# Performance work log

Hardware: AMD Instinct MI355X
Metric: run time of the kernel (lower is better)

## Reference

```python
import jax, jax.numpy as jnp
import numpy as np

H = W = 224
WS = 7          # window size
SS = 3          # shift size
NH = 12         # num heads
N = WS * WS     # tokens per window (49)


def _attn_mask():
    # shift-window attention mask, computed from static ints (numpy)
    img = np.zeros((H, W), np.float32)
    cnt = 0
    for h0, h1 in [(0, H - WS), (H - WS, H - SS), (H - SS, H)]:
        for w0, w1 in [(0, W - WS), (W - WS, W - SS), (W - SS, W)]:
            img[h0:h1, w0:w1] = cnt
            cnt += 1
    mw = img.reshape(H // WS, WS, W // WS, WS).transpose(0, 2, 1, 3).reshape(-1, N)
    diff = mw[:, None, :] - mw[:, :, None]          # (nW, N, N)
    m = np.where(diff != 0, -100.0, 0.0).astype(np.float32)
    return m[:, None, :, :]                         # (nW, 1, N, N)


def _rel_pos_index():
    coords = np.stack(np.meshgrid(np.arange(WS), np.arange(WS), indexing='ij'))
    cf = coords.reshape(2, -1)
    rc = (cf[:, :, None] - cf[:, None, :]).transpose(1, 2, 0)  # (N, N, 2)
    rc[..., 0] += WS - 1
    rc[..., 1] += WS - 1
    rc[..., 0] *= 2 * WS - 1
    return rc.sum(-1).reshape(-1)                    # (N*N,)


_MASK = _attn_mask()
_RPI = _rel_pos_index()


def _ln(x, w, b, eps=1e-5):
    mu = jnp.mean(x, -1, keepdims=True)
    var = jnp.mean((x - mu) ** 2, -1, keepdims=True)
    return (x - mu) / jnp.sqrt(var + eps) * w + b


def setup_inputs() -> dict:
    key = jax.random.key(0)
    ks = jax.random.split(key, 12)
    C, CM = 384, 1536
    s = 0.02
    return {
        'x': jax.random.normal(ks[0], (1, H * W, C), jnp.float32),
        'rpb_table': jax.random.normal(ks[1], (169, NH), jnp.float32) * s,
        'qkv_w': jax.random.normal(ks[2], (3 * C, C), jnp.float32) * s,
        'qkv_b': jax.random.normal(ks[3], (3 * C,), jnp.float32) * s,
        'proj_w': jax.random.normal(ks[4], (C, C), jnp.float32) * s,
        'proj_b': jax.random.normal(ks[5], (C,), jnp.float32) * s,
        'fc1_w': jax.random.normal(ks[6], (CM, C), jnp.float32) * s,
        'fc1_b': jax.random.normal(ks[7], (CM,), jnp.float32) * s,
        'fc2_w': jax.random.normal(ks[8], (C, CM), jnp.float32) * s,
        'fc2_b': jax.random.normal(ks[9], (C,), jnp.float32) * s,
        'norm1_w': jnp.ones((C,), jnp.float32),
        'norm1_b': jnp.zeros((C,), jnp.float32),
        'norm2_w': jnp.ones((C,), jnp.float32),
        'norm2_b': jnp.zeros((C,), jnp.float32),
    }


def reference(x, rpb_table, qkv_w, qkv_b, proj_w, proj_b, fc1_w, fc1_b,
              fc2_w, fc2_b, norm1_w, norm1_b, norm2_w, norm2_b):
    B, L, C = x.shape
    hd = C // NH
    scale = hd ** -0.5
    mask = jnp.asarray(_MASK)                        # (nW, 1, N, N)
    rpi = jnp.asarray(_RPI)

    shortcut = x
    h = _ln(x, norm1_w, norm1_b).reshape(B, H, W, C)
    h = jnp.roll(h, (-SS, -SS), axis=(1, 2))
    # window partition -> (B*nW, N, C)
    win = h.reshape(B, H // WS, WS, W // WS, WS, C).transpose(0, 1, 3, 2, 4, 5)
    win = win.reshape(-1, N, C)

    qkv = (win @ qkv_w.T + qkv_b).reshape(-1, N, 3, NH, hd).transpose(2, 0, 3, 1, 4)
    q, k, v = qkv[0] * scale, qkv[1], qkv[2]         # (nW, NH, N, hd)
    attn = jnp.einsum('whnd,whmd->whnm', q, k)
    bias = rpb_table[rpi].reshape(N, N, NH).transpose(2, 0, 1)[None]  # (1, NH, N, N)
    attn = jax.nn.softmax(attn + bias + mask, axis=-1)
    out = jnp.einsum('whnm,whmd->whnd', attn, v).transpose(0, 2, 1, 3).reshape(-1, N, C)
    out = out @ proj_w.T + proj_b

    # window reverse + unshift
    h = out.reshape(B, H // WS, W // WS, WS, WS, C).transpose(0, 1, 3, 2, 4, 5)
    h = h.reshape(B, H, W, C)
    h = jnp.roll(h, (SS, SS), axis=(1, 2)).reshape(B, L, C)

    x = shortcut + h
    y = _ln(x, norm2_w, norm2_b)
    y = jax.nn.gelu(y @ fc1_w.T + fc1_b, approximate=False)  # torch nn.GELU = erf
    y = y @ fc2_w.T + fc2_b
    return x + y
```

## Files before the change

### kernel.cpp

```cpp
#include <hip/hip_runtime.h>
#include <cstdint>
#include <cstddef>

#define AS1 __attribute__((address_space(1)))
#define AS3 __attribute__((address_space(3)))

typedef __attribute__((ext_vector_type(8))) short bf16x8;
typedef __attribute__((ext_vector_type(4))) short short4v;
typedef __attribute__((ext_vector_type(8))) unsigned short u16x8;
typedef __attribute__((ext_vector_type(4))) float f32x4;
typedef __attribute__((ext_vector_type(4))) unsigned short u16x4;

__device__ __forceinline__ float b2f(uint16_t u){ return __uint_as_float(((uint32_t)u) << 16); }
__device__ __forceinline__ uint16_t f2b(float f){
    uint32_t u = __float_as_uint(f);
    return (uint16_t)((u + 0x7fffu + ((u >> 16) & 1u)) >> 16);
}

__device__ __forceinline__ int pixof(int r){
    int w  = r / 49, t = r - w * 49;
    int wh = w >> 5, ww = w & 31;
    int th = t / 7,  tw = t - th * 7;
    int hp = wh * 7 + th + 3; if (hp >= 224) hp -= 224;
    int wp = ww * 7 + tw + 3; if (wp >= 224) wp -= 224;
    return hp * 224 + wp;
}

__global__ void f2b4_kernel(const float* __restrict__ a0, const float* __restrict__ a1,
                            const float* __restrict__ a2, const float* __restrict__ a3,
                            uint16_t* __restrict__ o0, uint16_t* __restrict__ o1,
                            uint16_t* __restrict__ o2, uint16_t* __restrict__ o3){
    int b = blockIdx.x;
    const float* src; uint16_t* dst; int base;
    if (b < 1728)      { src = a0; dst = o0; base = b; }
    else if (b < 2304) { src = a1; dst = o1; base = b - 1728; }
    else if (b < 4608) { src = a2; dst = o2; base = b - 2304; }
    else               { src = a3; dst = o3; base = b - 4608; }
    int i = base * 256 + threadIdx.x;
    dst[i] = f2b(src[i]);
}

__global__ void bm_init(const float* __restrict__ rpb, float* __restrict__ bm){
    int th = blockIdx.x;
    int type = th / 12, h = th - (th / 12) * 12;
    int eh = type >> 1, ew = type & 1;
    for (int idx = threadIdx.x; idx < 4096; idx += 256){
        int q = idx >> 6, kt = idx & 63;
        float v = 0.f;
        if (q < 49 && kt < 49){
            int ih = q / 7,  iw = q - 7 * (q / 7);
            int jh = kt / 7, jw = kt - 7 * (kt / 7);
            v = rpb[((ih - jh + 6) * 13 + (iw - jw + 6)) * 12 + h];
            int ri = (eh ? (ih < 4 ? 1 : 2) : 0) * 3 + (ew ? (iw < 4 ? 1 : 2) : 0);
            int rj = (eh ? (jh < 4 ? 1 : 2) : 0) * 3 + (ew ? (jw < 4 ? 1 : 2) : 0);
            if (ri != rj) v -= 100.f;
        }
        bm[(size_t)th * 4096 + idx] = v;
    }
}

template<int PERM>
__global__ __launch_bounds__(256) void ln_kernel(const float* __restrict__ in,
        const float* __restrict__ g, const float* __restrict__ b, uint16_t* __restrict__ out){
    int wave = threadIdx.x >> 6, lane = threadIdx.x & 63;
    int r = blockIdx.x * 4 + wave;
    int p = PERM ? pixof(r) : r;
    const float* row = in + (size_t)p * 384;
    float a[6];
    #pragma unroll
    for (int i = 0; i < 6; ++i) a[i] = row[lane * 6 + i];
    float s = 0.f, q = 0.f;
    #pragma unroll
    for (int i = 0; i < 6; ++i){ s += a[i]; q += a[i] * a[i]; }
    #pragma unroll
    for (int o = 32; o; o >>= 1){ s += __shfl_xor(s, o); q += __shfl_xor(q, o); }
    float mu   = s * (1.f / 384.f);
    float var  = q * (1.f / 384.f) - mu * mu;
    float rstd = rsqrtf(var + 1e-5f);
    uint16_t* orow = out + (size_t)r * 384;
    #pragma unroll
    for (int i = 0; i < 6; ++i){
        int c = lane * 6 + i;
        orow[c] = f2b((a[i] - mu) * rstd * g[c] + b[c]);
    }
}

template<int EPI>
__global__ __launch_bounds__(256, 2) void gemm_bt(
        const uint16_t* __restrict__ A, const uint16_t* __restrict__ B,
        const float* __restrict__ bias, void* __restrict__ outp,
        const float* __restrict__ xres, int N, int K, int row0)
{
    __shared__ alignas(16) uint16_t lA[128 * 64];
    __shared__ alignas(16) uint16_t lB[128 * 64];
    int tid  = threadIdx.x;
    int lane = tid & 63, wave = tid >> 6;

    int nwg = gridDim.x, bid = blockIdx.x;
    int q8 = nwg >> 3, r8 = nwg & 7;
    int xcd = bid & 7, idx = bid >> 3;
    int wg = (xcd < r8 ? xcd * (q8 + 1) : r8 * (q8 + 1) + (xcd - r8) * q8) + idx;

    int nt = N >> 7;
    int bm = wg / nt, bn = wg - bm * nt;
    int wr = wave >> 1, wc = wave & 1;
    int fr = lane & 15, kc = lane >> 4;

    int srow = wave * 32 + (lane >> 3);
    int cs   = (lane & 7) ^ ((lane >> 3) & 7);
    const uint16_t* gA = A + (size_t)(bm * 128 + srow) * K + cs * 8;
    const uint16_t* gB = B + (size_t)(bn * 128 + srow) * K + cs * 8;

    int aoff[4], boff[4];
    #pragma unroll
    for (int m = 0; m < 4; ++m){
        int row = wr * 64 + m * 16 + fr;
        aoff[m] = row * 128 + ((kc * 16) ^ ((row & 7) << 4));
        int rowB = wc * 64 + m * 16 + fr;
        boff[m] = rowB * 128 + ((kc * 16) ^ ((rowB & 7) << 4));
    }

    f32x4 acc[4][4] = {};
    const int NT = K >> 6;
    for (int t = 0; t < NT; ++t){
        int k0 = t << 6;
        #pragma unroll
        for (int it = 0; it < 4; ++it){
            __builtin_amdgcn_global_load_lds((const AS1 void*)(gA + k0 + (size_t)it * 8 * K),
                (AS3 void*)((AS3 char*)lA + wave * 4096 + it * 1024), 16, 0, 0);
            __builtin_amdgcn_global_load_lds((const AS1 void*)(gB + k0 + (size_t)it * 8 * K),
                (AS3 void*)((AS3 char*)lB + wave * 4096 + it * 1024), 16, 0, 0);
        }
        __syncthreads();

        #pragma unroll
        for (int ks = 0; ks < 2; ++ks){
            bf16x8 af[4], bv[4];
            #pragma unroll
            for (int m = 0; m < 4; ++m)
                af[m] = *(const bf16x8*)((const char*)lA + (aoff[m] ^ (ks << 6)));
            #pragma unroll
            for (int n = 0; n < 4; ++n)
                bv[n] = *(const bf16x8*)((const char*)lB + (boff[n] ^ (ks << 6)));
            #pragma unroll
            for (int m = 0; m < 4; ++m)
                #pragma unroll
                for (int n = 0; n < 4; ++n)
                    acc[m][n] = __builtin_amdgcn_mfma_f32_16x16x32_bf16(af[m], bv[n], acc[m][n], 0, 0, 0);
        }
        __syncthreads();
    }

    int colb = bn * 128 + wc * 64 + fr;
    int rowb = bm * 128 + wr * 64 + ((lane >> 4) << 2);
    float bvv[4];
    #pragma unroll
    for (int n = 0; n < 4; ++n) bvv[n] = bias[colb + n * 16];

    if constexpr (EPI == 0 || EPI == 1 || EPI == 5){
        uint16_t* out = (uint16_t*)outp;
        #pragma unroll
        for (int m = 0; m < 4; ++m)
            #pragma unroll
            for (int rg = 0; rg < 4; ++rg){
                size_t rr = (size_t)(rowb + m * 16 + rg) * N;
                #pragma unroll
                for (int n = 0; n < 4; ++n){
                    int col = colb + n * 16;
                    float v = acc[m][n][rg] + bvv[n];
                    if constexpr (EPI == 1) v = 0.5f * v * (1.f + erff(v * 0.7071067811865475f));
                    if constexpr (EPI == 5){ if (col < 384) v *= 0.1767766952966369f; }
                    out[rr + col] = f2b(v);
                }
            }
    } else if constexpr (EPI == 2){
        float* out = (float*)outp;
        #pragma unroll
        for (int m = 0; m < 4; ++m)
            #pragma unroll
            for (int rg = 0; rg < 4; ++rg){
                int r = row0 + rowb + m * 16 + rg;
                size_t pb = (size_t)pixof(r) * 384;
                #pragma unroll
                for (int n = 0; n < 4; ++n){
                    int c = colb + n * 16;
                    out[pb + c] = xres[pb + c] + acc[m][n][rg] + bvv[n];
                }
            }
    } else {
        float* out = (float*)outp;
        #pragma unroll
        for (int m = 0; m < 4; ++m)
            #pragma unroll
            for (int rg = 0; rg < 4; ++rg){
                size_t rb2 = (size_t)(rowb + m * 16 + rg) * 384;
                #pragma unroll
                for (int n = 0; n < 4; ++n){
                    int c = colb + n * 16;
                    out[rb2 + c] = out[rb2 + c] + acc[m][n][rg] + bvv[n];
                }
            }
    }
}

__global__ __launch_bounds__(256) void attn_mfma(const uint16_t* __restrict__ qkv,
        const float* __restrict__ bm, uint16_t* __restrict__ out)
{
    __shared__ uint16_t vtl[4][32][68];
    int wv = threadIdx.x >> 6, lane = threadIdx.x & 63;
    int p = blockIdx.x * 4 + wv;
    int w = p / 12, h = p - w * 12;
    int c = lane & 15, g = lane >> 4;
    const uint16_t* base = qkv + (size_t)(w * 49) * 1152 + h * 32;

    u16x8 vreg[4];
    #pragma unroll
    for (int it = 0; it < 4; ++it){
        int u = it * 64 + lane;
        int t = u >> 2, dq = u & 3;
        u16x8 v8 = {0,0,0,0,0,0,0,0};
        if (t < 49) v8 = *(const u16x8*)(base + (size_t)t * 1152 + 768 + dq * 8);
        vreg[it] = v8;
    }

    bf16x8 qf[4], kf[4];
    #pragma unroll
    for (int nt = 0; nt < 4; ++nt) qf[nt] = *(const bf16x8*)(base + (size_t)(16 * nt + c) * 1152 + g * 8);
    #pragma unroll
    for (int mt = 0; mt < 4; ++mt) kf[mt] = *(const bf16x8*)(base + (size_t)(16 * mt + c) * 1152 + 384 + g * 8);

    int wh = w >> 5, ww = w & 31;
    int type = ((wh == 31) << 1) | (ww == 31);
    const float* bmp = bm + (size_t)(type * 12 + h) * 4096;
    f32x4 sv[4][4];
    __builtin_amdgcn_s_setprio(1);
    #pragma unroll
    for (int mt = 0; mt < 4; ++mt)
        #pragma unroll
        for (int nt = 0; nt < 4; ++nt){
            f32x4 cb = *(const f32x4*)(bmp + (16 * nt + c) * 64 + 16 * mt + 4 * g);
            sv[mt][nt] = __builtin_amdgcn_mfma_f32_16x16x32_bf16(kf[mt], qf[nt], cb, 0, 0, 0);
        }
    __builtin_amdgcn_s_setprio(0);

    #pragma unroll
    for (int it = 0; it < 4; ++it){
        int u = it * 64 + lane;
        int t = u >> 2, dq = u & 3;
        #pragma unroll
        for (int j = 0; j < 8; ++j) vtl[wv][dq * 8 + j][t] = vreg[it][j];
    }

    #pragma unroll
    for (int nt = 0; nt < 4; ++nt)
        #pragma unroll
        for (int r = 0; r < 4; ++r)
            if (4 * g + r >= 1) sv[3][nt][r] = -1e9f;

    float inv[4];
    #pragma unroll
    for (int nt = 0; nt < 4; ++nt){
        float mx = -1e30f;
        #pragma unroll
        for (int mt = 0; mt < 4; ++mt)
            #pragma unroll
            for (int r = 0; r < 4; ++r) mx = fmaxf(mx, sv[mt][nt][r]);
        mx = fmaxf(mx, __shfl_xor(mx, 16));
        mx = fmaxf(mx, __shfl_xor(mx, 32));
        float sum = 0.f;
        #pragma unroll
        for (int mt = 0; mt < 4; ++mt)
            #pragma unroll
            for (int r = 0; r < 4; ++r){
                float e = __expf(sv[mt][nt][r] - mx);
                sv[mt][nt][r] = e; sum += e;
            }
        sum += __shfl_xor(sum, 16);
        sum += __shfl_xor(sum, 32);
        inv[nt] = 1.f / sum;
    }

    unsigned pk[4][4][2];
    #pragma unroll
    for (int nt = 0; nt < 4; ++nt)
        #pragma unroll
        for (int mt = 0; mt < 4; ++mt)
            #pragma unroll
            for (int pr = 0; pr < 2; ++pr)
                pk[nt][mt][pr] = (unsigned)f2b(sv[mt][nt][2 * pr]) |
                                 ((unsigned)f2b(sv[mt][nt][2 * pr + 1]) << 16);

    int a0 = (c + 16 * (2 * (g & 1))) * 4;
    int a1 = a0 + 64;
    int sel = g >> 1;

    f32x4 acco[2][4] = {};
    #pragma unroll
    for (int ks = 0; ks < 2; ++ks){
        bf16x8 va[2];
        #pragma unroll
        for (int mt = 0; mt < 2; ++mt){
            short4v lo = *(const short4v*)&vtl[wv][mt * 16 + c][ks * 32 + g * 8];
            short4v hi = *(const short4v*)&vtl[wv][mt * 16 + c][ks * 32 + g * 8 + 4];
            bf16x8 t;
            t[0] = lo[0]; t[1] = lo[1]; t[2] = lo[2]; t[3] = lo[3];
            t[4] = hi[0]; t[5] = hi[1]; t[6] = hi[2]; t[7] = hi[3];
            va[mt] = t;
        }
        bf16x8 pb[4];
        #pragma unroll
        for (int nt = 0; nt < 4; ++nt){
            union { unsigned u[4]; bf16x8 v; } pbu;
            #pragma unroll
            for (int t = 0; t < 4; ++t){
                int addr = (t >> 1) ? a1 : a0;
                unsigned lo2 = (unsigned)__builtin_amdgcn_ds_bpermute(addr, (int)pk[nt][2 * ks][t & 1]);
                unsigned hi2 = (unsigned)__builtin_amdgcn_ds_bpermute(addr, (int)pk[nt][2 * ks + 1][t & 1]);
                pbu.u[t] = sel ? hi2 : lo2;
            }
            pb[nt] = pbu.v;
        }
        __builtin_amdgcn_s_setprio(1);
        #pragma unroll
        for (int nt = 0; nt < 4; ++nt)
            #pragma unroll
            for (int mt = 0; mt < 2; ++mt)
                acco[mt][nt] = __builtin_amdgcn_mfma_f32_16x16x32_bf16(va[mt], pb[nt], acco[mt][nt], 0, 0, 0);
        __builtin_amdgcn_s_setprio(0);
    }

    #pragma unroll
    for (int mt = 0; mt < 2; ++mt)
        #pragma unroll
        for (int nt = 0; nt < 4; ++nt){
            int q = 16 * nt + c;
            if (q < 49){
                u16x4 o;
                #pragma unroll
                for (int r = 0; r < 4; ++r) o[r] = f2b(acco[mt][nt][r] * inv[nt]);
                *(u16x4*)(out + (size_t)(w * 49 + q) * 384 + h * 32 + 16 * mt + 4 * g) = o;
            }
        }
}

extern "C" void kernel_launch(void* const* d_in, const int* in_sizes, int n_in,
                              void* d_out, int out_size, void* d_ws, size_t ws_size,
                              hipStream_t stream) {
    const float* x      = (const float*)d_in[0];
    const float* rpb    = (const float*)d_in[1];
    const float* qkv_w  = (const float*)d_in[2];
    const float* qkv_b  = (const float*)d_in[3];
    const float* proj_w = (const float*)d_in[4];
    const float* proj_b = (const float*)d_in[5];
    const float* fc1_w  = (const float*)d_in[6];
    const float* fc1_b  = (const float*)d_in[7];
    const float* fc2_w  = (const float*)d_in[8];
    const float* fc2_b  = (const float*)d_in[9];
    const float* n1w    = (const float*)d_in[10];
    const float* n1b    = (const float*)d_in[11];
    const float* n2w    = (const float*)d_in[12];
    const float* n2b    = (const float*)d_in[13];

    char* ws = (char*)d_ws;
    uint16_t* winA = (uint16_t*)ws;
    uint16_t* qkB  = (uint16_t*)(ws + 38535168);
    uint16_t* wbuf = (uint16_t*)(ws + 154140672);
    uint16_t* w_qkv  = wbuf;
    uint16_t* w_proj = wbuf + 442368;
    uint16_t* w_fc1  = w_proj + 147456;
    uint16_t* w_fc2  = w_fc1 + 589824;
    float*    bmtab  = (float*)(ws + 157679616);

    f2b4_kernel<<<6912, 256, 0, stream>>>(qkv_w, proj_w, fc1_w, fc2_w,
                                          w_qkv, w_proj, w_fc1, w_fc2);
    bm_init<<<48, 256, 0, stream>>>(rpb, bmtab);

    ln_kernel<1><<<12544, 256, 0, stream>>>(x, n1w, n1b, winA);

    gemm_bt<5><<<392 * 9, 256, 0, stream>>>(winA, w_qkv, qkv_b, qkB, nullptr, 1152, 384, 0);

    attn_mfma<<<3072, 256, 0, stream>>>(qkB, bmtab, winA);

    gemm_bt<2><<<392 * 3, 256, 0, stream>>>(winA, w_proj, proj_b, d_out, x, 384, 384, 0);

    ln_kernel<0><<<12544, 256, 0, stream>>>((const float*)d_out, n2w, n2b, winA);

    for (int c2 = 0; c2 < 2; ++c2){
        size_t r0 = (size_t)c2 * 25088;
        gemm_bt<1><<<196 * 12, 256, 0, stream>>>(winA + r0 * 384, w_fc1, fc1_b, qkB, nullptr, 1536, 384, 0);
        gemm_bt<3><<<196 * 3, 256, 0, stream>>>(qkB, w_fc2, fc2_b, (float*)d_out + r0 * 384, nullptr, 384, 1536, 0);
    }
}
```

Before: 381.4 us.

## Store post-attention residual in bf16 and fold bias-mask init into weight conversion

The proj GEMM epilogue now writes the residual sum x+attn as bf16 into a scratch buffer instead of fp32 into the output. LayerNorm2 reads that bf16 buffer with 16-byte vector loads. The fc2 epilogue reads the bf16 residual, so it no longer does a read-modify-write of fp32 output. The bias/mask table init is merged into the weight-conversion kernel to save one launch, and the MLP hidden activations get their own buffer. This cuts memory traffic on the residual path, at the cost of rounding the residual stream to bf16, which lowers accuracy of the final output.

```diff
diff --git a/kernel.cpp b/kernel.cpp
--- a/kernel.cpp
+++ b/kernel.cpp
@@ -26,11 +26,31 @@
     return hp * 224 + wp;
 }
 
-__global__ void f2b4_kernel(const float* __restrict__ a0, const float* __restrict__ a1,
+__global__ void f2bm_kernel(const float* __restrict__ a0, const float* __restrict__ a1,
                             const float* __restrict__ a2, const float* __restrict__ a3,
                             uint16_t* __restrict__ o0, uint16_t* __restrict__ o1,
-                            uint16_t* __restrict__ o2, uint16_t* __restrict__ o3){
+                            uint16_t* __restrict__ o2, uint16_t* __restrict__ o3,
+                            const float* __restrict__ rpb, float* __restrict__ bm){
     int b = blockIdx.x;
+    if (b >= 6912){
+        int th = b - 6912;
+        int type = th / 12, h = th - (th / 12) * 12;
+        int eh = type >> 1, ew = type & 1;
+        for (int idx = threadIdx.x; idx < 4096; idx += 256){
+            int q = idx >> 6, kt = idx & 63;
+            float v = 0.f;
+            if (q < 49 && kt < 49){
+                int ih = q / 7,  iw = q - 7 * (q / 7);
+                int jh = kt / 7, jw = kt - 7 * (kt / 7);
+                v = rpb[((ih - jh + 6) * 13 + (iw - jw + 6)) * 12 + h];
+                int ri = (eh ? (ih < 4 ? 1 : 2) : 0) * 3 + (ew ? (iw < 4 ? 1 : 2) : 0);
+                int rj = (eh ? (jh < 4 ? 1 : 2) : 0) * 3 + (ew ? (jw < 4 ? 1 : 2) : 0);
+                if (ri != rj) v -= 100.f;
+            }
+            bm[(size_t)th * 4096 + idx] = v;
+        }
+        return;
+    }
     const float* src; uint16_t* dst; int base;
     if (b < 1728)      { src = a0; dst = o0; base = b; }
     else if (b < 2304) { src = a1; dst = o1; base = b - 1728; }
@@ -40,31 +60,11 @@
     dst[i] = f2b(src[i]);
 }
 
-__global__ void bm_init(const float* __restrict__ rpb, float* __restrict__ bm){
-    int th = blockIdx.x;
-    int type = th / 12, h = th - (th / 12) * 12;
-    int eh = type >> 1, ew = type & 1;
-    for (int idx = threadIdx.x; idx < 4096; idx += 256){
-        int q = idx >> 6, kt = idx & 63;
-        float v = 0.f;
-        if (q < 49 && kt < 49){
-            int ih = q / 7,  iw = q - 7 * (q / 7);
-            int jh = kt / 7, jw = kt - 7 * (kt / 7);
-            v = rpb[((ih - jh + 6) * 13 + (iw - jw + 6)) * 12 + h];
-            int ri = (eh ? (ih < 4 ? 1 : 2) : 0) * 3 + (ew ? (iw < 4 ? 1 : 2) : 0);
-            int rj = (eh ? (jh < 4 ? 1 : 2) : 0) * 3 + (ew ? (jw < 4 ? 1 : 2) : 0);
-            if (ri != rj) v -= 100.f;
-        }
-        bm[(size_t)th * 4096 + idx] = v;
-    }
-}
-
-template<int PERM>
 __global__ __launch_bounds__(256) void ln_kernel(const float* __restrict__ in,
         const float* __restrict__ g, const float* __restrict__ b, uint16_t* __restrict__ out){
     int wave = threadIdx.x >> 6, lane = threadIdx.x & 63;
     int r = blockIdx.x * 4 + wave;
-    int p = PERM ? pixof(r) : r;
+    int p = pixof(r);
     const float* row = in + (size_t)p * 384;
     float a[6];
     #pragma unroll
@@ -85,11 +85,38 @@
     }
 }
 
+__global__ __launch_bounds__(256) void ln2_kernel(const uint16_t* __restrict__ in,
+        const float* __restrict__ g, const float* __restrict__ b, uint16_t* __restrict__ out){
+    int wave = threadIdx.x >> 6, lane = threadIdx.x & 63;
+    int r = blockIdx.x * 4 + wave;
+    u16x8 v8 = {0,0,0,0,0,0,0,0};
+    if (lane < 48) v8 = *(const u16x8*)(in + (size_t)r * 384 + lane * 8);
+    float a[8];
+    float s = 0.f, q = 0.f;
+    #pragma unroll
+    for (int i = 0; i < 8; ++i){ a[i] = b2f(v8[i]); s += a[i]; q += a[i] * a[i]; }
+    #pragma unroll
+    for (int o = 32; o; o >>= 1){ s += __shfl_xor(s, o); q += __shfl_xor(q, o); }
+    float mu   = s * (1.f / 384.f);
+    float var  = q * (1.f / 384.f) - mu * mu;
+    float rstd = rsqrtf(var + 1e-5f);
+    if (lane < 48){
+        u16x8 o8;
+        #pragma unroll
+        for (int i = 0; i < 8; ++i){
+            int c = lane * 8 + i;
+            o8[i] = f2b((a[i] - mu) * rstd * g[c] + b[c]);
+        }
+        *(u16x8*)(out + (size_t)r * 384 + lane * 8) = o8;
+    }
+}
+
 template<int EPI>
 __global__ __launch_bounds__(256, 2) void gemm_bt(
         const uint16_t* __restrict__ A, const uint16_t* __restrict__ B,
         const float* __restrict__ bias, void* __restrict__ outp,
-        const float* __restrict__ xres, int N, int K, int row0)
+        const float* __restrict__ xres, const uint16_t* __restrict__ xb,
+        int N, int K, int row0)
 {
     __shared__ alignas(16) uint16_t lA[128 * 64];
     __shared__ alignas(16) uint16_t lB[128 * 64];
@@ -157,7 +184,7 @@
     #pragma unroll
     for (int n = 0; n < 4; ++n) bvv[n] = bias[colb + n * 16];
 
-    if constexpr (EPI == 0 || EPI == 1 || EPI == 5){
+    if constexpr (EPI == 1 || EPI == 5){
         uint16_t* out = (uint16_t*)outp;
         #pragma unroll
         for (int m = 0; m < 4; ++m)
@@ -173,8 +200,8 @@
                     out[rr + col] = f2b(v);
                 }
             }
-    } else if constexpr (EPI == 2){
-        float* out = (float*)outp;
+    } else if constexpr (EPI == 6){
+        uint16_t* out = (uint16_t*)outp;
         #pragma unroll
         for (int m = 0; m < 4; ++m)
             #pragma unroll
@@ -184,7 +211,7 @@
                 #pragma unroll
                 for (int n = 0; n < 4; ++n){
                     int c = colb + n * 16;
-                    out[pb + c] = xres[pb + c] + acc[m][n][rg] + bvv[n];
+                    out[pb + c] = f2b(xres[pb + c] + acc[m][n][rg] + bvv[n]);
                 }
             }
     } else {
@@ -197,7 +224,7 @@
                 #pragma unroll
                 for (int n = 0; n < 4; ++n){
                     int c = colb + n * 16;
-                    out[rb2 + c] = out[rb2 + c] + acc[m][n][rg] + bvv[n];
+                    out[rb2 + c] = b2f(xb[rb2 + c]) + acc[m][n][rg] + bvv[n];
                 }
             }
     }
@@ -362,32 +389,33 @@
     const float* n2b    = (const float*)d_in[13];
 
     char* ws = (char*)d_ws;
-    uint16_t* winA = (uint16_t*)ws;
-    uint16_t* qkB  = (uint16_t*)(ws + 38535168);
-    uint16_t* wbuf = (uint16_t*)(ws + 154140672);
+    uint16_t* winA  = (uint16_t*)ws;
+    uint16_t* qkB   = (uint16_t*)(ws + 38535168);
+    uint16_t* x2b   = qkB;
+    uint16_t* hid   = (uint16_t*)(ws + 77070336);
+    uint16_t* wbuf  = (uint16_t*)(ws + 154140672);
     uint16_t* w_qkv  = wbuf;
     uint16_t* w_proj = wbuf + 442368;
     uint16_t* w_fc1  = w_proj + 147456;
     uint16_t* w_fc2  = w_fc1 + 589824;
     float*    bmtab  = (float*)(ws + 157679616);
 
-    f2b4_kernel<<<6912, 256, 0, stream>>>(qkv_w, proj_w, fc1_w, fc2_w,
-                                          w_qkv, w_proj, w_fc1, w_fc2);
-    bm_init<<<48, 256, 0, stream>>>(rpb, bmtab);
-
-    ln_kernel<1><<<12544, 256, 0, stream>>>(x, n1w, n1b, winA);
-
-    gemm_bt<5><<<392 * 9, 256, 0, stream>>>(winA, w_qkv, qkv_b, qkB, nullptr, 1152, 384, 0);
+    f2bm_kernel<<<6960, 256, 0, stream>>>(qkv_w, proj_w, fc1_w, fc2_w,
+                                          w_qkv, w_proj, w_fc1, w_fc2, rpb, bmtab);
+
+    ln_kernel<<<12544, 256, 0, stream>>>(x, n1w, n1b, winA);
+
+    gemm_bt<5><<<392 * 9, 256, 0, stream>>>(winA, w_qkv, qkv_b, qkB, nullptr, nullptr, 1152, 384, 0);
 
     attn_mfma<<<3072, 256, 0, stream>>>(qkB, bmtab, winA);
 
-    gemm_bt<2><<<392 * 3, 256, 0, stream>>>(winA, w_proj, proj_b, d_out, x, 384, 384, 0);
-
-    ln_kernel<0><<<12544, 256, 0, stream>>>((const float*)d_out, n2w, n2b, winA);
+    gemm_bt<6><<<392 * 3, 256, 0, stream>>>(winA, w_proj, proj_b, x2b, x, nullptr, 384, 384, 0);
+
+    ln2_kernel<<<12544, 256, 0, stream>>>(x2b, n2w, n2b, winA);
 
     for (int c2 = 0; c2 < 2; ++c2){
         size_t r0 = (size_t)c2 * 25088;
-        gemm_bt<1><<<196 * 12, 256, 0, stream>>>(winA + r0 * 384, w_fc1, fc1_b, qkB, nullptr, 1536, 384, 0);
-        gemm_bt<3><<<196 * 3, 256, 0, stream>>>(qkB, w_fc2, fc2_b, (float*)d_out + r0 * 384, nullptr, 384, 1536, 0);
-    }
-}
+        gemm_bt<1><<<196 * 12, 256, 0, stream>>>(winA + r0 * 384, w_fc1, fc1_b, hid, nullptr, nullptr, 1536, 384, 0);
+        gemm_bt<7><<<196 * 3, 256, 0, stream>>>(hid, w_fc2, fc2_b, (float*)d_out + r0 * 384, nullptr, x2b + r0 * 384, 384, 1536, 0);
+    }
+}
```

New measurement: 348.6 us. 1.09x faster.
